# Kernel optimization log

Hardware: AMD Instinct MI355X
Metric: run time of the kernel (lower is better)

The kernel has to match this reference:

```python
import jax, jax.numpy as jnp
import numpy as np

VLAD_K = 8   # vlad_cluster
GHOST = 2    # ghost_cluster
EPS = 1e-12  # F.normalize eps


def setup_inputs() -> dict:
    key = jax.random.key(0)
    k1, k2, k3, k4 = jax.random.split(key, 4)
    N, C, H, W = 32, 512, 16, 32
    KG = VLAD_K + GHOST
    x = jax.random.normal(k1, (N, C, H, W), dtype=jnp.float32)
    conv_w = jax.random.normal(k2, (KG, C), dtype=jnp.float32) * 0.05  # 1x1 conv weight
    conv_b = jax.random.normal(k3, (KG,), dtype=jnp.float32) * 0.05
    centers = jax.random.uniform(k4, (KG, C), dtype=jnp.float32)
    return {"x": x, "conv_w": conv_w, "conv_b": conv_b, "centers": centers}


def _l2norm(v, axis):
    n = jnp.sqrt(jnp.sum(v * v, axis=axis, keepdims=True))
    return v / jnp.maximum(n, EPS)


def reference(x, conv_w, conv_b, centers):
    N, C, H, W = x.shape
    L = H * W
    xf = x.reshape(N, C, L)  # [N, C, HW]
    # 1x1 conv -> logits [N, K+G, HW], softmax over cluster dim
    logits = jnp.einsum('kc,ncl->nkl', conv_w, xf) + conv_b[None, :, None]
    a = jax.nn.softmax(logits, axis=1)
    # sum_l a[n,k,l]*(x[n,c,l] - centers[k,c]) decomposed into two small matmuls
    assign_x = jnp.einsum('nkl,ncl->nkc', a, xf)          # [N, K+G, C]
    assign_sum = jnp.sum(a, axis=-1)                      # [N, K+G]
    cluster_res = assign_x - assign_sum[:, :, None] * centers[None]
    cluster_res = cluster_res[:, :VLAD_K, :]              # drop ghost clusters
    cluster_res = _l2norm(cluster_res, axis=-1)           # intra-norm
    vlad = cluster_res.reshape(N, -1)                     # [N, K*C]
    return _l2norm(vlad, axis=-1)
```

## Files before the change

kernel.cpp:

```cpp
#include <hip/hip_runtime.h>

#define N_   32
#define C_   512
#define L_   512
#define KG_  10
#define K_   8
#define LCH  8
#define LT   64
#define XP   65
#define RP   11
#define EPSF 1e-12f

__global__ __launch_bounds__(512, 2) void k_main(
    const float* __restrict__ x, const float* __restrict__ cw,
    const float* __restrict__ cb, float* __restrict__ part,
    float* __restrict__ asum_part)
{
    __shared__ float xs[C_ * XP];
    __shared__ float red[8][LT][RP];
    __shared__ float a_s[LT][K_];

    const int n   = blockIdx.x;
    const int ch  = blockIdx.y;
    const int tid = threadIdx.x;

    const float* xbase = x + (size_t)n * C_ * L_ + ch * LT;
#pragma unroll
    for (int j = 0; j < 16; ++j) {
        const int it = tid + j * 512;
        const int c = it >> 4, q = it & 15;
        const float4 v = *reinterpret_cast<const float4*>(xbase + (size_t)c * L_ + q * 4);
        const int b = c * XP + q * 4;
        xs[b]     = v.x;
        xs[b + 1] = v.y;
        xs[b + 2] = v.z;
        xs[b + 3] = v.w;
    }
    __syncthreads();

    const int l  = tid & 63;
    const int cg = tid >> 6;
    const int c0 = __builtin_amdgcn_readfirstlane(cg) << 6;

    float acc[KG_];
#pragma unroll
    for (int k = 0; k < KG_; ++k) acc[k] = 0.f;

#pragma unroll
    for (int h = 0; h < 4; ++h) {
        const int cbase = c0 + h * 16;
        float xr[16];
#pragma unroll
        for (int ci = 0; ci < 16; ++ci)
            xr[ci] = xs[(cbase + ci) * XP + l];
#pragma unroll
        for (int k = 0; k < KG_; ++k) {
            const float* w = cw + k * C_ + cbase;
#pragma unroll
            for (int ci = 0; ci < 16; ++ci)
                acc[k] = fmaf(w[ci], xr[ci], acc[k]);
        }
    }

#pragma unroll
    for (int k = 0; k < KG_; ++k) red[cg][l][k] = acc[k];
    __syncthreads();

    for (int idx = tid; idx < LT * KG_; idx += 512) {
        const int li = idx / KG_, k = idx - li * KG_;
        float s = red[0][li][k];
#pragma unroll
        for (int g = 1; g < 8; ++g) s += red[g][li][k];
        red[0][li][k] = s;
    }
    __syncthreads();

    if (tid < LT) {
        float v[KG_];
        float m = -1e30f;
#pragma unroll
        for (int k = 0; k < KG_; ++k) {
            v[k] = red[0][tid][k] + cb[k];
            m = fmaxf(m, v[k]);
        }
        float s = 0.f;
#pragma unroll
        for (int k = 0; k < KG_; ++k) { v[k] = __expf(v[k] - m); s += v[k]; }
        const float inv = 1.f / s;
#pragma unroll
        for (int k = 0; k < K_; ++k) {
            const float av = v[k] * inv;
            a_s[tid][k] = av;
            float t = av;
#pragma unroll
            for (int off = 32; off > 0; off >>= 1) t += __shfl_down(t, off);
            if (tid == 0)
                asum_part[((size_t)n * LCH + ch) * K_ + k] = t;
        }
    }
    __syncthreads();

    const int c = tid;
    float bacc[K_];
#pragma unroll
    for (int k = 0; k < K_; ++k) bacc[k] = 0.f;

#pragma unroll 4
    for (int li = 0; li < LT; ++li) {
        const float xv = xs[c * XP + li];
        const float4 a0 = *reinterpret_cast<const float4*>(&a_s[li][0]);
        const float4 a1 = *reinterpret_cast<const float4*>(&a_s[li][4]);
        bacc[0] = fmaf(a0.x, xv, bacc[0]);
        bacc[1] = fmaf(a0.y, xv, bacc[1]);
        bacc[2] = fmaf(a0.z, xv, bacc[2]);
        bacc[3] = fmaf(a0.w, xv, bacc[3]);
        bacc[4] = fmaf(a1.x, xv, bacc[4]);
        bacc[5] = fmaf(a1.y, xv, bacc[5]);
        bacc[6] = fmaf(a1.z, xv, bacc[6]);
        bacc[7] = fmaf(a1.w, xv, bacc[7]);
    }

    float* pp = part + (((size_t)n * LCH + ch) * K_) * C_ + c;
#pragma unroll
    for (int k = 0; k < K_; ++k)
        pp[(size_t)k * C_] = bacc[k];
}

__global__ __launch_bounds__(256) void k_final(
    const float* __restrict__ part, const float* __restrict__ asum_part,
    const float* __restrict__ centers, float* __restrict__ out)
{
    const int n    = blockIdx.x;
    const int tid  = threadIdx.x;
    const int lane = tid & 63;
    const int wv   = tid >> 6;

    __shared__ float s_asum[K_];
    __shared__ float s_inv[K_];
    __shared__ float s_q[K_];
    __shared__ float s_ginv;
    __shared__ float wred[4][K_];

    if (tid < K_) {
        float s = 0.f;
#pragma unroll
        for (int c2 = 0; c2 < LCH; ++c2)
            s += asum_part[((size_t)n * LCH + c2) * K_ + tid];
        s_asum[tid] = s;
    }
    __syncthreads();

    float r[K_][2];
    float ssq[K_];
#pragma unroll
    for (int k = 0; k < K_; ++k) ssq[k] = 0.f;

#pragma unroll
    for (int j = 0; j < 2; ++j) {
        const int c = tid + j * 256;
#pragma unroll
        for (int k = 0; k < K_; ++k) {
            float v = 0.f;
#pragma unroll
            for (int c2 = 0; c2 < LCH; ++c2)
                v += part[(((size_t)n * LCH + c2) * K_ + k) * C_ + c];
            v -= s_asum[k] * centers[k * C_ + c];
            r[k][j] = v;
            ssq[k] += v * v;
        }
    }

#pragma unroll
    for (int k = 0; k < K_; ++k) {
        float t = ssq[k];
#pragma unroll
        for (int off = 32; off > 0; off >>= 1) t += __shfl_down(t, off);
        if (lane == 0) wred[wv][k] = t;
    }
    __syncthreads();

    if (tid < K_) {
        const float t = wred[0][tid] + wred[1][tid] + wred[2][tid] + wred[3][tid];
        const float inv = 1.f / fmaxf(sqrtf(t), EPSF);
        s_inv[tid] = inv;
        s_q[tid]   = t * inv * inv;
    }
    __syncthreads();

    if (tid == 0) {
        float g = 0.f;
#pragma unroll
        for (int k = 0; k < K_; ++k) g += s_q[k];
        s_ginv = 1.f / fmaxf(sqrtf(g), EPSF);
    }
    __syncthreads();

    const float ginv = s_ginv;
#pragma unroll
    for (int j = 0; j < 2; ++j) {
        const int c = tid + j * 256;
#pragma unroll
        for (int k = 0; k < K_; ++k)
            out[(size_t)n * (K_ * C_) + k * C_ + c] = r[k][j] * s_inv[k] * ginv;
    }
}

extern "C" void kernel_launch(void* const* d_in, const int* in_sizes, int n_in,
                              void* d_out, int out_size, void* d_ws, size_t ws_size,
                              hipStream_t stream)
{
    const float* x       = (const float*)d_in[0];
    const float* conv_w  = (const float*)d_in[1];
    const float* conv_b  = (const float*)d_in[2];
    const float* centers = (const float*)d_in[3];
    float* out = (float*)d_out;

    float* part      = (float*)d_ws;
    float* asum_part = part + (size_t)N_ * LCH * K_ * C_;

    dim3 grid(N_, LCH);
    hipLaunchKernelGGL(k_main, grid, dim3(512), 0, stream,
                       x, conv_w, conv_b, part, asum_part);
    hipLaunchKernelGGL(k_final, dim3(N_), dim3(256), 0, stream,
                       part, asum_part, centers, out);
}
```

Measured before the change: 95.54 us.

## Split x tile load into halves to overlap logits compute with second half

The main kernel now issues all global loads for the x tile up front into registers. It stores only the first half of the channels to shared memory and computes the partial logits over that half while the second half's loads are still in flight, then stores and processes the second half. This is meant to hide global load latency behind compute, at the cost of many more live registers (16 float4), which may hurt occupancy under launch_bounds(512,2). Separately, the final kernel moves to 512 threads, one channel per thread, to raise parallelism in the small reduction kernel.

```diff
diff --git a/kernel.cpp b/kernel.cpp
--- a/kernel.cpp
+++ b/kernel.cpp
@@ -23,32 +23,69 @@
     const int n   = blockIdx.x;
     const int ch  = blockIdx.y;
     const int tid = threadIdx.x;
+    const int l   = tid & 63;
+    const int cg  = tid >> 6;
 
     const float* xbase = x + (size_t)n * C_ * L_ + ch * LT;
-#pragma unroll
-    for (int j = 0; j < 16; ++j) {
+
+    float4 v0[8], v1[8];
+#pragma unroll
+    for (int j = 0; j < 8; ++j) {
         const int it = tid + j * 512;
         const int c = it >> 4, q = it & 15;
-        const float4 v = *reinterpret_cast<const float4*>(xbase + (size_t)c * L_ + q * 4);
+        v0[j] = *reinterpret_cast<const float4*>(xbase + (size_t)c * L_ + q * 4);
+    }
+#pragma unroll
+    for (int j = 0; j < 8; ++j) {
+        const int it = tid + j * 512;
+        const int c = (it >> 4) + 256, q = it & 15;
+        v1[j] = *reinterpret_cast<const float4*>(xbase + (size_t)c * L_ + q * 4);
+    }
+
+#pragma unroll
+    for (int j = 0; j < 8; ++j) {
+        const int it = tid + j * 512;
+        const int c = it >> 4, q = it & 15;
         const int b = c * XP + q * 4;
-        xs[b]     = v.x;
-        xs[b + 1] = v.y;
-        xs[b + 2] = v.z;
-        xs[b + 3] = v.w;
-    }
-    __syncthreads();
-
-    const int l  = tid & 63;
-    const int cg = tid >> 6;
-    const int c0 = __builtin_amdgcn_readfirstlane(cg) << 6;
+        xs[b] = v0[j].x; xs[b + 1] = v0[j].y; xs[b + 2] = v0[j].z; xs[b + 3] = v0[j].w;
+    }
+    __syncthreads();
+
+    const int c0 = __builtin_amdgcn_readfirstlane(cg) << 5;
 
     float acc[KG_];
 #pragma unroll
     for (int k = 0; k < KG_; ++k) acc[k] = 0.f;
 
 #pragma unroll
-    for (int h = 0; h < 4; ++h) {
+    for (int h = 0; h < 2; ++h) {
         const int cbase = c0 + h * 16;
+        float xr[16];
+#pragma unroll
+        for (int ci = 0; ci < 16; ++ci)
+            xr[ci] = xs[(cbase + ci) * XP + l];
+#pragma unroll
+        for (int k = 0; k < KG_; ++k) {
+            const float* w = cw + k * C_ + cbase;
+#pragma unroll
+            for (int ci = 0; ci < 16; ++ci)
+                acc[k] = fmaf(w[ci], xr[ci], acc[k]);
+        }
+    }
+
+#pragma unroll
+    for (int j = 0; j < 8; ++j) {
+        const int it = tid + j * 512;
+        const int c = (it >> 4) + 256, q = it & 15;
+        const int b = c * XP + q * 4;
+        xs[b] = v1[j].x; xs[b + 1] = v1[j].y; xs[b + 2] = v1[j].z; xs[b + 3] = v1[j].w;
+    }
+    __syncthreads();
+
+    const int c1 = 256 + c0;
+#pragma unroll
+    for (int h = 0; h < 2; ++h) {
+        const int cbase = c1 + h * 16;
         float xr[16];
 #pragma unroll
         for (int ci = 0; ci < 16; ++ci)
@@ -126,7 +163,7 @@
         pp[(size_t)k * C_] = bacc[k];
 }
 
-__global__ __launch_bounds__(256) void k_final(
+__global__ __launch_bounds__(512) void k_final(
     const float* __restrict__ part, const float* __restrict__ asum_part,
     const float* __restrict__ centers, float* __restrict__ out)
 {
@@ -139,7 +176,7 @@
     __shared__ float s_inv[K_];
     __shared__ float s_q[K_];
     __shared__ float s_ginv;
-    __shared__ float wred[4][K_];
+    __shared__ float wred[8][K_];
 
     if (tid < K_) {
         float s = 0.f;
@@ -150,24 +187,18 @@
     }
     __syncthreads();
 
-    float r[K_][2];
+    const int c = tid;
+    float r[K_];
     float ssq[K_];
 #pragma unroll
-    for (int k = 0; k < K_; ++k) ssq[k] = 0.f;
-
-#pragma unroll
-    for (int j = 0; j < 2; ++j) {
-        const int c = tid + j * 256;
-#pragma unroll
-        for (int k = 0; k < K_; ++k) {
-            float v = 0.f;
-#pragma unroll
-            for (int c2 = 0; c2 < LCH; ++c2)
-                v += part[(((size_t)n * LCH + c2) * K_ + k) * C_ + c];
-            v -= s_asum[k] * centers[k * C_ + c];
-            r[k][j] = v;
-            ssq[k] += v * v;
-        }
+    for (int k = 0; k < K_; ++k) {
+        float v = 0.f;
+#pragma unroll
+        for (int c2 = 0; c2 < LCH; ++c2)
+            v += part[(((size_t)n * LCH + c2) * K_ + k) * C_ + c];
+        v -= s_asum[k] * centers[k * C_ + c];
+        r[k] = v;
+        ssq[k] = v * v;
     }
 
 #pragma unroll
@@ -180,7 +211,9 @@
     __syncthreads();
 
     if (tid < K_) {
-        const float t = wred[0][tid] + wred[1][tid] + wred[2][tid] + wred[3][tid];
+        float t = 0.f;
+#pragma unroll
+        for (int w = 0; w < 8; ++w) t += wred[w][tid];
         const float inv = 1.f / fmaxf(sqrtf(t), EPSF);
         s_inv[tid] = inv;
         s_q[tid]   = t * inv * inv;
@@ -197,12 +230,8 @@
 
     const float ginv = s_ginv;
 #pragma unroll
-    for (int j = 0; j < 2; ++j) {
-        const int c = tid + j * 256;
-#pragma unroll
-        for (int k = 0; k < K_; ++k)
-            out[(size_t)n * (K_ * C_) + k * C_ + c] = r[k][j] * s_inv[k] * ginv;
-    }
+    for (int k = 0; k < K_; ++k)
+        out[(size_t)n * (K_ * C_) + k * C_ + c] = r[k] * s_inv[k] * ginv;
 }
 
 extern "C" void kernel_launch(void* const* d_in, const int* in_sizes, int n_in,
@@ -221,6 +250,6 @@
     dim3 grid(N_, LCH);
     hipLaunchKernelGGL(k_main, grid, dim3(512), 0, stream,
                        x, conv_w, conv_b, part, asum_part);
-    hipLaunchKernelGGL(k_final, dim3(N_), dim3(256), 0, stream,
+    hipLaunchKernelGGL(k_final, dim3(N_), dim3(512), 0, stream,
                        part, asum_part, centers, out);
 }
```

Result: faster. 93.40 us (-2.2%).
